# Performance work log

Hardware: AMD Instinct MI355X
Metric: run time of the kernel (lower is better)

## Reference

```python
import jax, jax.numpy as jnp
import numpy as np

N_NODES = 100000
N_EDGES = 1600000
D_FEAT = 64
D_HID = 128
N_HOP = 3


def setup_inputs() -> dict:
    key = jax.random.key(0)
    ks = jax.random.split(key, 7)
    nodes = jax.random.normal(ks[0], (N_NODES, D_FEAT), dtype=jnp.float32)
    senders = jax.random.randint(ks[1], (N_EDGES,), 0, N_NODES, dtype=jnp.int32)
    receivers = jax.random.randint(ks[2], (N_EDGES,), 0, N_NODES, dtype=jnp.int32)
    # per-hop MLP params (n_hop=3 independent layers), lecun-style scaling
    W1 = jax.random.normal(ks[3], (N_HOP, D_FEAT, D_HID), dtype=jnp.float32) / np.sqrt(D_FEAT)
    b1 = jnp.zeros((N_HOP, D_HID), dtype=jnp.float32)
    W2 = jax.random.normal(ks[4], (N_HOP, D_HID, D_FEAT), dtype=jnp.float32) / np.sqrt(D_HID)
    b2 = jnp.zeros((N_HOP, D_FEAT), dtype=jnp.float32)
    return {"nodes": nodes, "senders": senders, "receivers": receivers,
            "W1": W1, "b1": b1, "W2": W2, "b2": b2}


def _gcn_hop(x, senders, receivers, w1, b1, w2, b2):
    # update_node_fn: 2-layer MLP with leaky_relu between layers
    x = jax.nn.leaky_relu(jnp.dot(x, w1) + b1)
    x = jnp.dot(x, w2) + b2
    n = x.shape[0]
    ones = jnp.ones(senders.shape, dtype=x.dtype)
    send_deg = jax.ops.segment_sum(ones, senders, num_segments=n)
    recv_deg = jax.ops.segment_sum(ones, receivers, num_segments=n)
    # symmetric normalization: D_s^{-1/2} gather -> scatter-sum -> D_r^{-1/2}
    x = x * jax.lax.rsqrt(jnp.maximum(send_deg, 1.0))[:, None]
    x = jax.ops.segment_sum(x[senders], receivers, num_segments=n)
    x = x * jax.lax.rsqrt(jnp.maximum(recv_deg, 1.0))[:, None]
    return x


def reference(nodes, senders, receivers, W1, b1, W2, b2):
    x = nodes
    for i in range(N_HOP):
        x = _gcn_hop(x, senders, receivers, W1[i], b1[i], W2[i], b2[i])
    return x
```

## Files before the change

kernel.cpp:

```cpp
#include <hip/hip_runtime.h>

#define LRELU_SLOPE 0.01f
#define NBLK_A 512
#define BIN_SZ 256
#define MAXBIN 5120
#define NC2 64

typedef unsigned short ushort_t;
typedef unsigned int uint_t;

typedef float f32x4 __attribute__((ext_vector_type(4)));
typedef short bf16x8 __attribute__((ext_vector_type(8)));
#define MFMA16(a, b, c) __builtin_amdgcn_mfma_f32_16x16x32_bf16(a, b, c, 0, 0, 0)

__device__ inline uint_t f2bf(float f) {
    unsigned u = __float_as_uint(f);
    return (u + 0x7FFFu + ((u >> 16) & 1u)) >> 16;
}

__device__ inline void split2(float v, uint_t& hi, uint_t& lo) {
    hi = f2bf(v);
    float hif = __uint_as_float(hi << 16);
    lo = f2bf(v - hif);
}

__device__ inline float4 bf4_to_f4(ushort4 v) {
    float4 r;
    r.x = __uint_as_float((unsigned)v.x << 16);
    r.y = __uint_as_float((unsigned)v.y << 16);
    r.z = __uint_as_float((unsigned)v.z << 16);
    r.w = __uint_as_float((unsigned)v.w << 16);
    return r;
}


__global__ __launch_bounds__(256) void binhist_kernel(const int* __restrict__ keys,
        int* __restrict__ cntA, int cs, int e, int nbins) {
    __shared__ int cnt[512];
    int b = blockIdx.x, t = threadIdx.x;
    for (int i = t; i < nbins; i += 256) cnt[i] = 0;
    __syncthreads();
    int base = b * cs, lim = min(cs, e - base);
    for (int i = t; i < lim; i += 256)
        atomicAdd(&cnt[keys[base + i] >> 8], 1);
    __syncthreads();
    for (int i = t; i < nbins; i += 256) cntA[b * nbins + i] = cnt[i];
}

__global__ __launch_bounds__(512) void bintot_kernel(const int* __restrict__ cntA,
        int* __restrict__ binStart, int nbins) {
    __shared__ int s[512];
    int t = threadIdx.x;
    int v = 0;
    if (t < nbins)
        for (int b = 0; b < NBLK_A; b++) v += cntA[b * nbins + t];
    s[t] = v;
    __syncthreads();
    for (int off = 1; off < 512; off <<= 1) {
        int add = (t >= off) ? s[t - off] : 0;
        __syncthreads();
        s[t] += add;
        __syncthreads();
    }
    if (t < nbins) binStart[t] = s[t] - v;
    if (t == nbins - 1) binStart[nbins] = s[t];
}

__global__ __launch_bounds__(512) void binoff_kernel(const int* __restrict__ cntA,
        const int* __restrict__ binStart, int* __restrict__ offT, int nbins) {
    __shared__ int s[NBLK_A];
    int bin = blockIdx.x, t = threadIdx.x;
    int v = cntA[t * nbins + bin];
    s[t] = v;
    __syncthreads();
    for (int off = 1; off < NBLK_A; off <<= 1) {
        int add = (t >= off) ? s[t - off] : 0;
        __syncthreads();
        s[t] += add;
        __syncthreads();
    }
    offT[bin * NBLK_A + t] = binStart[bin] + s[t] - v;
}

__global__ __launch_bounds__(256) void binscat_kernel(const int* __restrict__ keys,
        const int* __restrict__ payload, const int* __restrict__ offT,
        uint2* __restrict__ pairs, int cs, int e, int nbins) {
    __shared__ int cur[512];
    int b = blockIdx.x, t = threadIdx.x;
    for (int i = t; i < nbins; i += 256) cur[i] = offT[i * NBLK_A + b];
    __syncthreads();
    int base = b * cs, lim = min(cs, e - base);
    for (int i = t; i < lim; i += 256) {
        int k = keys[base + i];
        int pl = payload[base + i];
        int pos = atomicAdd(&cur[k >> 8], 1);
        pairs[pos] = make_uint2((unsigned)k, (unsigned)pl);
    }
}

__global__ __launch_bounds__(256) void binsort_kernel(const uint2* __restrict__ pairs,
        const int* __restrict__ binStart, int* __restrict__ row_start,
        int* __restrict__ bucket, int nbins, int n, int e) {
    __shared__ int cnt[BIN_SZ];
    __shared__ int loc[BIN_SZ];
    __shared__ int buf[MAXBIN];
    int bin = blockIdx.x, t = threadIdx.x;
    int e0 = binStart[bin], e1 = binStart[bin + 1];
    int m = e1 - e0;
    if (m > MAXBIN) m = MAXBIN;
    cnt[t] = 0;
    __syncthreads();
    for (int i = t; i < m; i += 256)
        atomicAdd(&cnt[pairs[e0 + i].x & 255], 1);
    __syncthreads();
    int v = cnt[t];
    int node = bin * BIN_SZ + t;
    loc[t] = v;
    __syncthreads();
    for (int off = 1; off < BIN_SZ; off <<= 1) {
        int add = (t >= off) ? loc[t - off] : 0;
        __syncthreads();
        loc[t] += add;
        __syncthreads();
    }
    int excl = loc[t] - v;
    if (node < n) row_start[node] = e0 + excl;
    if (bin == nbins - 1 && t == 255) row_start[n] = e;
    cnt[t] = excl;
    __syncthreads();
    for (int i = t; i < m; i += 256) {
        uint2 pr = pairs[e0 + i];
        int pos = atomicAdd(&cnt[pr.x & 255], 1);
        buf[pos] = (int)pr.y;
    }
    __syncthreads();
    for (int i = t; i < m; i += 256) bucket[e0 + i] = buf[i];
}


__global__ __launch_bounds__(256) void hist8v2_kernel(const int* __restrict__ keys,
        uint_t* __restrict__ hist, int cs, int e, int half, int nwords) {
    __shared__ uint_t lds[12500];
    int c = blockIdx.x >> 1;
    int h = blockIdx.x & 1;
    int t = threadIdx.x;
    int hw = half >> 2;
    for (int i = t; i < hw; i += 256) lds[i] = 0;
    __syncthreads();
    int base = c * cs, lim = min(cs, e - base);
    int lo = h * half;
    for (int i = t; i < lim; i += 256) {
        int v = keys[base + i] - lo;
        if ((unsigned)v < (unsigned)half)
            atomicAdd(&lds[v >> 2], 1u << ((v & 3) * 8));
    }
    __syncthreads();
    uint_t* d = hist + (size_t)c * nwords + (size_t)h * hw;
    for (int i = t; i < hw; i += 256) d[i] = lds[i];
}

__global__ __launch_bounds__(256) void scancv2_kernel(const uint_t* __restrict__ hist,
        int* __restrict__ deg, int nwords, int n) {
    int w = blockIdx.x * 256 + threadIdx.x;
    if (w >= nwords) return;
    uint_t run = 0;
    for (int c = 0; c < NC2; c++) run += hist[(size_t)c * nwords + w];
    int v = w * 4;
    if (v + 3 < n) {
        ((int4*)deg)[w] = make_int4(run & 255, (run >> 8) & 255,
                                    (run >> 16) & 255, (int)(run >> 24));
    } else {
        for (int j = 0; j < 4 && v + j < n; j++) deg[v + j] = (run >> (8 * j)) & 255;
    }
}


__global__ __launch_bounds__(256) void prep_w_kernel(const float* __restrict__ W1,
        const float* __restrict__ W2, ushort_t* __restrict__ w1p, ushort_t* __restrict__ w2p) {
    int hop = blockIdx.x;
    const float* w1 = W1 + hop * 64 * 128;
    const float* w2 = W2 + hop * 128 * 64;
    ushort_t* p1h = w1p + (size_t)hop * 16384;
    ushort_t* p1l = p1h + 8192;
    ushort_t* p2h = w2p + (size_t)hop * 16384;
    ushort_t* p2l = p2h + 8192;
    for (int i = threadIdx.x; i < 8192; i += 256) {
        int j = i & 7, o = (i >> 3) & 127, cq = i >> 10;
        int k = (cq >> 2) * 32 + (cq & 3) * 8 + j;
        uint_t h, l;
        split2(w1[k * 128 + o], h, l);
        p1h[i] = (ushort_t)h; p1l[i] = (ushort_t)l;
    }
    for (int i = threadIdx.x; i < 8192; i += 256) {
        int j = i & 7, o = (i >> 3) & 63, cq = i >> 9;
        int k = (cq >> 2) * 32 + (cq & 3) * 8 + j;
        uint_t h, l;
        split2(w2[k * 64 + o], h, l);
        p2h[i] = (ushort_t)h; p2l[i] = (ushort_t)l;
    }
}


__global__ __launch_bounds__(512) void fused_mlp_kernel(const float* __restrict__ x,
        const ushort_t* __restrict__ w1p, const float* __restrict__ b1g,
        const ushort_t* __restrict__ w2p, const float* __restrict__ b2g,
        const int* __restrict__ sdeg, ushort_t* __restrict__ y, int n) {
    __shared__ __align__(16) char smem[54272];
    ushort_t* xsh = (ushort_t*)smem;
    ushort_t* xsl = xsh + 4608;
    ushort_t* hsh = xsl + 4608;
    ushort_t* hsl = hsh + 8704;
    float* b1f   = (float*)(hsl + 8704);
    float* b2f   = b1f + 128;
    float* snorm = b2f + 64;
    float* ybuf  = (float*)smem;

    const ushort_t* w1ph = w1p;
    const ushort_t* w1pl = w1p + 8192;
    const ushort_t* w2ph = w2p;
    const ushort_t* w2pl = w2p + 8192;

    int tid = threadIdx.x;
    int nb = blockIdx.x * 64;

    for (int i = tid; i < 1024; i += 512) {
        int node = i >> 4, c4 = i & 15;
        int gn = nb + node;
        float4 v = make_float4(0.f, 0.f, 0.f, 0.f);
        if (gn < n) v = ((const float4*)x)[(size_t)gn * 16 + c4];
        uint_t h0, l0, h1, l1, h2, l2, h3, l3;
        split2(v.x, h0, l0); split2(v.y, h1, l1);
        split2(v.z, h2, l2); split2(v.w, h3, l3);
        *(uint2*)&xsh[node * 72 + c4 * 4] = make_uint2(h0 | (h1 << 16), h2 | (h3 << 16));
        *(uint2*)&xsl[node * 72 + c4 * 4] = make_uint2(l0 | (l1 << 16), l2 | (l3 << 16));
    }
    if (tid < 32) ((float4*)b1f)[tid] = ((const float4*)b1g)[tid];
    else if (tid < 48) ((float4*)b2f)[tid - 32] = ((const float4*)b2g)[tid - 32];
    if (tid >= 448) {
        int t = tid - 448;
        int gn = nb + t;
        int d = (gn < n) ? sdeg[gn] : 1;
        snorm[t] = rsqrtf(fmaxf((float)d, 1.0f));
    }
    __syncthreads();

    int w = tid >> 6, lane = tid & 63;
    int q = lane >> 4, m = lane & 15;
    int oq = w & 3, nh = w >> 2;
    bool even = ((m & 1) == 0);

    {
        f32x4 acc[2][2];
        #pragma unroll
        for (int a = 0; a < 2; a++)
            #pragma unroll
            for (int b = 0; b < 2; b++) acc[a][b] = (f32x4)(0.f);

        #pragma unroll
        for (int c = 0; c < 2; c++) {
            bf16x8 Ah[2], Al[2];
            #pragma unroll
            for (int nt = 0; nt < 2; nt++) {
                int node = nh * 32 + nt * 16 + m;
                Ah[nt] = *(const bf16x8*)&xsh[node * 72 + c * 32 + q * 8];
                Al[nt] = *(const bf16x8*)&xsl[node * 72 + c * 32 + q * 8];
            }
            #pragma unroll
            for (int ot = 0; ot < 2; ot++) {
                int o1 = oq * 32 + ot * 16 + m;
                size_t fo = (size_t)((c * 4 + q) * 128 + o1) * 8;
                bf16x8 Bh = *(const bf16x8*)&w1ph[fo];
                bf16x8 Bl = *(const bf16x8*)&w1pl[fo];
                #pragma unroll
                for (int nt = 0; nt < 2; nt++) {
                    acc[ot][nt] = MFMA16(Ah[nt], Bh, acc[ot][nt]);
                    acc[ot][nt] = MFMA16(Ah[nt], Bl, acc[ot][nt]);
                    acc[ot][nt] = MFMA16(Al[nt], Bh, acc[ot][nt]);
                }
            }
        }
        float b1v[2];
        b1v[0] = b1f[oq * 32 + m];
        b1v[1] = b1f[oq * 32 + 16 + m];
        #pragma unroll
        for (int ot = 0; ot < 2; ot++)
            #pragma unroll
            for (int nt = 0; nt < 2; nt++) {
                float hv[4], pv[4];
                #pragma unroll
                for (int r = 0; r < 4; r++) {
                    float t = acc[ot][nt][r] + b1v[ot];
                    hv[r] = (t > 0.f) ? t : LRELU_SLOPE * t;
                }
                #pragma unroll
                for (int r = 0; r < 4; r++) pv[r] = __shfl_xor(hv[r], 1, 64);
                int kpos = oq * 32 + ot * 16 + (m & ~1);
                #pragma unroll
                for (int rr = 0; rr < 2; rr++) {
                    int r = even ? rr : (2 + rr);
                    float vlo = even ? hv[r] : pv[r];
                    float vhi = even ? pv[r] : hv[r];
                    uint_t ah, al, bh, bl;
                    split2(vlo, ah, al);
                    split2(vhi, bh, bl);
                    int node = nh * 32 + nt * 16 + 4 * q + r;
                    *(uint_t*)&hsh[node * 136 + kpos] = ah | (bh << 16);
                    *(uint_t*)&hsl[node * 136 + kpos] = al | (bl << 16);
                }
            }
    }
    __syncthreads();

    {
        int ot2 = oq;
        f32x4 acc2[2];
        acc2[0] = (f32x4)(0.f);
        acc2[1] = (f32x4)(0.f);
        #pragma unroll
        for (int c = 0; c < 4; c++) {
            int o2 = ot2 * 16 + m;
            size_t fo = (size_t)((c * 4 + q) * 64 + o2) * 8;
            bf16x8 Bh = *(const bf16x8*)&w2ph[fo];
            bf16x8 Bl = *(const bf16x8*)&w2pl[fo];
            #pragma unroll
            for (int nt = 0; nt < 2; nt++) {
                int node = nh * 32 + nt * 16 + m;
                bf16x8 Ah = *(const bf16x8*)&hsh[node * 136 + c * 32 + q * 8];
                bf16x8 Al = *(const bf16x8*)&hsl[node * 136 + c * 32 + q * 8];
                acc2[nt] = MFMA16(Ah, Bh, acc2[nt]);
                acc2[nt] = MFMA16(Ah, Bl, acc2[nt]);
                acc2[nt] = MFMA16(Al, Bh, acc2[nt]);
            }
        }
        float b2v = b2f[ot2 * 16 + m];
        #pragma unroll
        for (int nt = 0; nt < 2; nt++)
            #pragma unroll
            for (int r = 0; r < 4; r++) {
                int node = nh * 32 + nt * 16 + 4 * q + r;
                float sn = snorm[node];
                ybuf[node * 68 + ot2 * 16 + m] = (acc2[nt][r] + b2v) * sn;
            }
    }
    __syncthreads();

    {
        int node = tid >> 3, c8 = tid & 7;
        int gn = nb + node;
        if (gn < n) {
            const float* src = &ybuf[node * 68 + c8 * 8];
            float4 v0 = *(const float4*)src;
            float4 v1 = *(const float4*)(src + 4);
            uint4 o;
            o.x = f2bf(v0.x) | (f2bf(v0.y) << 16);
            o.y = f2bf(v0.z) | (f2bf(v0.w) << 16);
            o.z = f2bf(v1.x) | (f2bf(v1.y) << 16);
            o.w = f2bf(v1.z) | (f2bf(v1.w) << 16);
            ((uint4*)y)[(size_t)gn * 8 + c8] = o;
        }
    }
}


__global__ __launch_bounds__(256) void agg_kernel(const ushort_t* __restrict__ y,
        const int* __restrict__ rs, const int* __restrict__ bucket,
        float* __restrict__ dst, int n) {
    int wid  = (blockIdx.x * 256 + threadIdx.x) >> 6;
    int lane = threadIdx.x & 63;
    int nd   = lane >> 5;
    int slot = (lane >> 4) & 1;
    int f4   = lane & 15;
    int node = wid * 2 + nd;
    if (node >= n) return;
    int s0  = rs[node];
    int deg = rs[node + 1] - s0;
    const ushort4* y4 = (const ushort4*)y;
    float4 acc = make_float4(0.f, 0.f, 0.f, 0.f);
    for (int i = slot; i < deg; i += 16) {
        int idx[8]; float ok[8];
        #pragma unroll
        for (int j = 0; j < 8; j++) {
            int ii = i + 2 * j;
            bool v = ii < deg;
            idx[j] = bucket[v ? s0 + ii : s0];
            ok[j] = v ? 1.0f : 0.0f;
        }
        #pragma unroll
        for (int j = 0; j < 8; j++) {
            float4 v4 = bf4_to_f4(y4[(size_t)idx[j] * 16 + f4]);
            acc.x = fmaf(v4.x, ok[j], acc.x);
            acc.y = fmaf(v4.y, ok[j], acc.y);
            acc.z = fmaf(v4.z, ok[j], acc.z);
            acc.w = fmaf(v4.w, ok[j], acc.w);
        }
    }
    acc.x += __shfl_xor(acc.x, 16, 64);
    acc.y += __shfl_xor(acc.y, 16, 64);
    acc.z += __shfl_xor(acc.z, 16, 64);
    acc.w += __shfl_xor(acc.w, 16, 64);
    if (slot == 0) {
        float sc = rsqrtf(fmaxf((float)deg, 1.0f));
        acc.x *= sc; acc.y *= sc; acc.z *= sc; acc.w *= sc;
        ((float4*)dst)[(size_t)node * 16 + f4] = acc;
    }
}


extern "C" void kernel_launch(void* const* d_in, const int* in_sizes, int n_in,
                              void* d_out, int out_size, void* d_ws, size_t ws_size,
                              hipStream_t stream) {
    const float* nodes     = (const float*)d_in[0];
    const int*   senders   = (const int*)d_in[1];
    const int*   receivers = (const int*)d_in[2];
    const float* W1 = (const float*)d_in[3];
    const float* b1 = (const float*)d_in[4];
    const float* W2 = (const float*)d_in[5];
    const float* b2 = (const float*)d_in[6];

    int N = in_sizes[0] / 64;
    int E = in_sizes[1];
    int NBINS = (N + BIN_SZ - 1) / BIN_SZ;
    int CSA = (E + NBLK_A - 1) / NBLK_A;
    int CS2 = (E + NC2 - 1) / NC2;
    int HALF = ((N + 7) / 8) * 4;
    int NW2 = 2 * (HALF >> 2);

    char* p = (char*)d_ws;
    auto carve = [&](size_t bytes) -> char* {
        char* r = p;
        p += (bytes + 255) & ~(size_t)255;
        return r;
    };
    float*    xbuf = (float*)carve((size_t)N * 64 * 4);
    float*    hbuf = (float*)carve((size_t)N * 128 * 4);
    ushort_t* ybuf = (ushort_t*)carve((size_t)N * 64 * 2);
    int*      rs   = (int*)carve((size_t)(N + 1) * 4);
    int*      sdeg = (int*)carve((size_t)N * 4);
    int*      bucket = (int*)carve((size_t)E * 4);
    int*      binStart = (int*)carve((size_t)(NBINS + 1) * 4);
    ushort_t* w1p  = (ushort_t*)carve((size_t)3 * 16384 * 2);
    ushort_t* w2p  = (ushort_t*)carve((size_t)3 * 16384 * 2);
    char* q = (char*)hbuf;
    uint2* pairs = (uint2*)q;                 q += (size_t)E * 8;
    int*   cntA  = (int*)q;                   q += (size_t)NBLK_A * NBINS * 4;
    int*   offT  = (int*)q;
    uint_t* T1   = (uint_t*)pairs;

    prep_w_kernel<<<3, 256, 0, stream>>>(W1, W2, w1p, w2p);
    binhist_kernel<<<NBLK_A, 256, 0, stream>>>(receivers, cntA, CSA, E, NBINS);
    bintot_kernel<<<1, 512, 0, stream>>>(cntA, binStart, NBINS);
    binoff_kernel<<<NBINS, NBLK_A, 0, stream>>>(cntA, binStart, offT, NBINS);
    binscat_kernel<<<NBLK_A, 256, 0, stream>>>(receivers, senders, offT, pairs, CSA, E, NBINS);
    binsort_kernel<<<NBINS, 256, 0, stream>>>(pairs, binStart, rs, bucket, NBINS, N, E);
    hist8v2_kernel<<<NC2 * 2, 256, 0, stream>>>(senders, T1, CS2, E, HALF, NW2);
    scancv2_kernel<<<(NW2 + 255) / 256, 256, 0, stream>>>(T1, sdeg, NW2, N);

    int mbf = (N + 63) / 64;
    int agg_blocks = (N / 2 + 4) / 4 + 1;
    for (int hop = 0; hop < 3; hop++) {
        const float* xin = (hop == 0) ? nodes : xbuf;
        float* dst = (hop == 2) ? (float*)d_out : xbuf;
        fused_mlp_kernel<<<mbf, 512, 0, stream>>>(xin,
                w1p + (size_t)hop * 16384, b1 + hop * 128,
                w2p + (size_t)hop * 16384, b2 + hop * 64,
                sdeg, ybuf, N);
        agg_kernel<<<agg_blocks, 256, 0, stream>>>(ybuf, rs, bucket, dst, N);
    }
}
```

Before: 393.9 us.

## Fuse neighbor aggregation into the next hop's MLP kernel prologue

Hops 2 and 3 of the MLP kernel now gather their input directly. Each block sums its nodes' incoming bf16 messages via the CSR (rs/bucket) into shared memory, instead of reading an fp32 x buffer written by a separate agg kernel. This removes two agg launches and the fp32 write/read round trip of the intermediate features, with ping-pong bf16 y buffers. The trade-off is that the gather now runs with 8 threads per node inside a 512-thread MFMA block, which may reduce the latency hiding the standalone agg kernel had and puts the irregular load on the MLP's critical path.

```diff
diff --git a/kernel.cpp b/kernel.cpp
--- a/kernel.cpp
+++ b/kernel.cpp
@@ -31,6 +31,17 @@
     r.z = __uint_as_float((unsigned)v.z << 16);
     r.w = __uint_as_float((unsigned)v.w << 16);
     return r;
+}
+
+__device__ inline void acc_bf8(uint4 v, float* a) {
+    a[0] += __uint_as_float(v.x << 16);
+    a[1] += __uint_as_float(v.x & 0xFFFF0000u);
+    a[2] += __uint_as_float(v.y << 16);
+    a[3] += __uint_as_float(v.y & 0xFFFF0000u);
+    a[4] += __uint_as_float(v.z << 16);
+    a[5] += __uint_as_float(v.z & 0xFFFF0000u);
+    a[6] += __uint_as_float(v.w << 16);
+    a[7] += __uint_as_float(v.w & 0xFFFF0000u);
 }
 
 
@@ -201,7 +212,10 @@
 }
 
 
+template<int GATHER>
 __global__ __launch_bounds__(512) void fused_mlp_kernel(const float* __restrict__ x,
+        const ushort_t* __restrict__ yin, const int* __restrict__ rs,
+        const int* __restrict__ bucket,
         const ushort_t* __restrict__ w1p, const float* __restrict__ b1g,
         const ushort_t* __restrict__ w2p, const float* __restrict__ b2g,
         const int* __restrict__ sdeg, ushort_t* __restrict__ y, int n) {
@@ -223,17 +237,6 @@
     int tid = threadIdx.x;
     int nb = blockIdx.x * 64;
 
-    for (int i = tid; i < 1024; i += 512) {
-        int node = i >> 4, c4 = i & 15;
-        int gn = nb + node;
-        float4 v = make_float4(0.f, 0.f, 0.f, 0.f);
-        if (gn < n) v = ((const float4*)x)[(size_t)gn * 16 + c4];
-        uint_t h0, l0, h1, l1, h2, l2, h3, l3;
-        split2(v.x, h0, l0); split2(v.y, h1, l1);
-        split2(v.z, h2, l2); split2(v.w, h3, l3);
-        *(uint2*)&xsh[node * 72 + c4 * 4] = make_uint2(h0 | (h1 << 16), h2 | (h3 << 16));
-        *(uint2*)&xsl[node * 72 + c4 * 4] = make_uint2(l0 | (l1 << 16), l2 | (l3 << 16));
-    }
     if (tid < 32) ((float4*)b1f)[tid] = ((const float4*)b1g)[tid];
     else if (tid < 48) ((float4*)b2f)[tid - 32] = ((const float4*)b2g)[tid - 32];
     if (tid >= 448) {
@@ -241,6 +244,60 @@
         int gn = nb + t;
         int d = (gn < n) ? sdeg[gn] : 1;
         snorm[t] = rsqrtf(fmaxf((float)d, 1.0f));
+    }
+
+    if (GATHER) {
+        int node = tid >> 3, j = tid & 7;
+        int gn = nb + node;
+        float a[8];
+        #pragma unroll
+        for (int k = 0; k < 8; k++) a[k] = 0.f;
+        if (gn < n) {
+            int s0 = rs[gn];
+            int deg = rs[gn + 1] - s0;
+            const uint4* yrow = (const uint4*)yin;
+            int i = 0;
+            for (; i + 4 <= deg; i += 4) {
+                int i0 = bucket[s0 + i];
+                int i1 = bucket[s0 + i + 1];
+                int i2 = bucket[s0 + i + 2];
+                int i3 = bucket[s0 + i + 3];
+                uint4 v0 = yrow[(size_t)i0 * 8 + j];
+                uint4 v1 = yrow[(size_t)i1 * 8 + j];
+                uint4 v2 = yrow[(size_t)i2 * 8 + j];
+                uint4 v3 = yrow[(size_t)i3 * 8 + j];
+                acc_bf8(v0, a); acc_bf8(v1, a); acc_bf8(v2, a); acc_bf8(v3, a);
+            }
+            for (; i < deg; i++) {
+                uint4 v = yrow[(size_t)bucket[s0 + i] * 8 + j];
+                acc_bf8(v, a);
+            }
+            float sc = rsqrtf(fmaxf((float)deg, 1.0f));
+            #pragma unroll
+            for (int k = 0; k < 8; k++) a[k] *= sc;
+        }
+        uint_t h[8], l[8];
+        #pragma unroll
+        for (int k = 0; k < 8; k++) split2(a[k], h[k], l[k]);
+        uint4 oh, ol;
+        oh.x = h[0] | (h[1] << 16); oh.y = h[2] | (h[3] << 16);
+        oh.z = h[4] | (h[5] << 16); oh.w = h[6] | (h[7] << 16);
+        ol.x = l[0] | (l[1] << 16); ol.y = l[2] | (l[3] << 16);
+        ol.z = l[4] | (l[5] << 16); ol.w = l[6] | (l[7] << 16);
+        *(uint4*)&xsh[node * 72 + j * 8] = oh;
+        *(uint4*)&xsl[node * 72 + j * 8] = ol;
+    } else {
+        for (int i = tid; i < 1024; i += 512) {
+            int node = i >> 4, c4 = i & 15;
+            int gn = nb + node;
+            float4 v = make_float4(0.f, 0.f, 0.f, 0.f);
+            if (gn < n) v = ((const float4*)x)[(size_t)gn * 16 + c4];
+            uint_t h0, l0, h1, l1, h2, l2, h3, l3;
+            split2(v.x, h0, l0); split2(v.y, h1, l1);
+            split2(v.z, h2, l2); split2(v.w, h3, l3);
+            *(uint2*)&xsh[node * 72 + c4 * 4] = make_uint2(h0 | (h1 << 16), h2 | (h3 << 16));
+            *(uint2*)&xsl[node * 72 + c4 * 4] = make_uint2(l0 | (l1 << 16), l2 | (l3 << 16));
+        }
     }
     __syncthreads();
 
@@ -431,19 +488,18 @@
         p += (bytes + 255) & ~(size_t)255;
         return r;
     };
-    float*    xbuf = (float*)carve((size_t)N * 64 * 4);
-    float*    hbuf = (float*)carve((size_t)N * 128 * 4);
-    ushort_t* ybuf = (ushort_t*)carve((size_t)N * 64 * 2);
+    ushort_t* yA   = (ushort_t*)carve((size_t)N * 64 * 2);
+    ushort_t* yB   = (ushort_t*)carve((size_t)N * 64 * 2);
     int*      rs   = (int*)carve((size_t)(N + 1) * 4);
     int*      sdeg = (int*)carve((size_t)N * 4);
     int*      bucket = (int*)carve((size_t)E * 4);
     int*      binStart = (int*)carve((size_t)(NBINS + 1) * 4);
     ushort_t* w1p  = (ushort_t*)carve((size_t)3 * 16384 * 2);
     ushort_t* w2p  = (ushort_t*)carve((size_t)3 * 16384 * 2);
-    char* q = (char*)hbuf;
-    uint2* pairs = (uint2*)q;                 q += (size_t)E * 8;
-    int*   cntA  = (int*)q;                   q += (size_t)NBLK_A * NBINS * 4;
-    int*   offT  = (int*)q;
+    char* scratch  = carve((size_t)E * 8 + 2 * (size_t)NBLK_A * NBINS * 4 + 1024);
+    uint2* pairs = (uint2*)scratch;
+    int*   cntA  = (int*)(scratch + (size_t)E * 8);
+    int*   offT  = cntA + (size_t)NBLK_A * NBINS;
     uint_t* T1   = (uint_t*)pairs;
 
     prep_w_kernel<<<3, 256, 0, stream>>>(W1, W2, w1p, w2p);
@@ -457,13 +513,12 @@
 
     int mbf = (N + 63) / 64;
     int agg_blocks = (N / 2 + 4) / 4 + 1;
-    for (int hop = 0; hop < 3; hop++) {
-        const float* xin = (hop == 0) ? nodes : xbuf;
-        float* dst = (hop == 2) ? (float*)d_out : xbuf;
-        fused_mlp_kernel<<<mbf, 512, 0, stream>>>(xin,
-                w1p + (size_t)hop * 16384, b1 + hop * 128,
-                w2p + (size_t)hop * 16384, b2 + hop * 64,
-                sdeg, ybuf, N);
-        agg_kernel<<<agg_blocks, 256, 0, stream>>>(ybuf, rs, bucket, dst, N);
-    }
-}
+
+    fused_mlp_kernel<0><<<mbf, 512, 0, stream>>>(nodes, nullptr, nullptr, nullptr,
+            w1p, b1, w2p, b2, sdeg, yA, N);
+    fused_mlp_kernel<1><<<mbf, 512, 0, stream>>>(nullptr, yA, rs, bucket,
+            w1p + 16384, b1 + 128, w2p + 16384, b2 + 64, sdeg, yB, N);
+    fused_mlp_kernel<1><<<mbf, 512, 0, stream>>>(nullptr, yB, rs, bucket,
+            w1p + 32768, b1 + 256, w2p + 32768, b2 + 128, sdeg, yA, N);
+    agg_kernel<<<agg_blocks, 256, 0, stream>>>(yA, rs, bucket, (float*)d_out, N);
+}
```

Result: no change. 400.7 us (+1.7%).
